# Kernel optimization log

Measured on AMD Instinct MI355X. Metric: run time of the kernel, lower is better.

Reference implementation:

```python
import math
import jax, jax.numpy as jnp
import numpy as np

N_HEAD = 32
LAYER_NUMBER = 10  # cancels out: beta*alibi*L + alpha*QK^T*L = alibi + QK^T/sqrt(d)


def build_alibi(seq_len, n_head, dtype):
    # Faithful port of BLOOM's build_alibi_tensor -> [n_head, 1, seq_len]
    cp2 = 2 ** math.floor(math.log2(n_head))
    base = 2.0 ** (-(2.0 ** -(math.log2(cp2) - 3)))
    slopes = base ** np.arange(1, 1 + cp2)
    if cp2 != n_head:
        extra_base = 2.0 ** (-(2.0 ** -(math.log2(2 * cp2) - 3)))
        num_rem = min(cp2, n_head - cp2)
        slopes = np.concatenate([slopes, extra_base ** np.arange(1, 1 + 2 * num_rem, 2)])
    alibi = slopes[:, None, None] * np.arange(seq_len)[None, None, :]
    return jnp.asarray(alibi, dtype)


def setup_inputs() -> dict:
    key = jax.random.key(0)
    ks = jax.random.split(key, 6)
    B, S, H = 4, 1024, 4096
    return {
        "hidden_states": jax.random.normal(ks[0], (B, S, H), jnp.float32),
        "residual": jax.random.normal(ks[1], (B, S, H), jnp.float32),
        "qkv_w": jax.random.normal(ks[2], (3 * H, H), jnp.float32) * 0.02,
        "qkv_b": jnp.zeros((3 * H,), jnp.float32),
        "dense_w": jax.random.normal(ks[3], (H, H), jnp.float32) * 0.02,
        "dense_b": jnp.zeros((H,), jnp.float32),
    }


def reference(hidden_states, residual, qkv_w, qkv_b, dense_w, dense_b):
    B, S, H = hidden_states.shape
    nh = N_HEAD
    d = H // nh
    # fused qkv projection: [B,S,3H] -> [B,S,nh,3d] -> split
    mixed = (hidden_states @ qkv_w.T + qkv_b).reshape(B, S, nh, 3 * d)
    q, k, v = jnp.split(mixed, 3, axis=-1)  # each [B,S,nh,d]

    alibi = build_alibi(S, nh, hidden_states.dtype)  # [nh,1,S]
    # beta*alibi + alpha*QK^T, then *layer_number in scaled softmax == alibi + QK^T/sqrt(d)
    scores = jnp.einsum("bqhd,bkhd->bhqk", q, k) / math.sqrt(d) + alibi[None]  # [B,nh,S,S]

    causal = jnp.tril(jnp.ones((S, S), bool))  # [S,S], True = attend
    scores = jnp.where(causal, scores, jnp.asarray(-10000.0, scores.dtype))
    # softmax in fp32 (attention_softmax_in_fp32), then zero masked entries like *(~padded_causal_mask)
    probs = jax.nn.softmax(scores.astype(jnp.float32), axis=-1) * causal
    probs = probs.astype(v.dtype)

    ctx = jnp.einsum("bhqk,bkhd->bqhd", probs, v).reshape(B, S, H)
    out = ctx @ dense_w.T + dense_b + residual  # dropout_add with p=0 / eval
    return out
```

## Files before the change

### kernel.cpp

```cpp
#include <hip/hip_runtime.h>
#include <hip/hip_bf16.h>

typedef __attribute__((ext_vector_type(8))) short bf16x8;
typedef __attribute__((ext_vector_type(4))) short short4v;
typedef __attribute__((ext_vector_type(4))) float f32x4;

#define MFMA16(A, B, C) __builtin_amdgcn_mfma_f32_16x16x32_bf16((A), (B), (C), 0, 0, 0)
#define GLDS16(g, l)                                                            \
  __builtin_amdgcn_global_load_lds(                                             \
      (const __attribute__((address_space(1))) void*)(g),                       \
      (__attribute__((address_space(3))) void*)(l), 16, 0, 0)

__device__ __forceinline__ short f2bf(float f) {
  union { float f; unsigned u; } v; v.f = f;
  return (short)((v.u + 0x7fffu + ((v.u >> 16) & 1u)) >> 16);
}

__device__ __forceinline__ void blk_barrier() {
  asm volatile("" ::: "memory");
  __builtin_amdgcn_s_barrier();
  asm volatile("" ::: "memory");
}

__global__ __launch_bounds__(256) void cvt_kernel(const float* __restrict__ in,
                                                  short* __restrict__ out, int n4) {
  int i = blockIdx.x * 256 + threadIdx.x;
  const int stride = gridDim.x * 256;
  for (; i < n4; i += stride) {
    f32x4 v = ((const f32x4*)in)[i];
    short4v o;
    o[0] = f2bf(v[0]); o[1] = f2bf(v[1]); o[2] = f2bf(v[2]); o[3] = f2bf(v[3]);
    ((short4v*)out)[i] = o;
  }
}

__global__ __launch_bounds__(512, 2) void gemm_bt8(const short* __restrict__ A,
                                                   const short* __restrict__ B,
                                                   const float* __restrict__ bias,
                                                   const float* __restrict__ resid,
                                                   short* __restrict__ Cb,
                                                   float* __restrict__ Cf,
                                                   int Mtiles, int Nn, int K, int mode) {
  __shared__ short sA[2][2][8192];
  __shared__ short sB[2][2][8192];
  const int tid = threadIdx.x;
  const int w = tid >> 6, l = tid & 63;
  const int wm = w >> 2, wn = w & 3;
  const int fr = l & 15, g4 = l >> 4, sx = l & 7;

  const int nwg = gridDim.x;
  const int qq = nwg >> 3, rr = nwg & 7;
  const int xcd = blockIdx.x & 7, sub = blockIdx.x >> 3;
  const int swz = (xcd < rr ? xcd * (qq + 1) : rr * (qq + 1) + (xcd - rr) * qq) + sub;
  const int rowBase = (swz % Mtiles) * 256;
  const int colBase = (swz / Mtiles) * 256;

  const int NT = K >> 6;
  const int swcol = ((l & 7) ^ (l >> 3)) * 8;
  const short* Ag = A + (size_t)(rowBase + w * 8 + (l >> 3)) * K + swcol;
  const short* Bg = B + (size_t)(colBase + w * 8 + (l >> 3)) * K + swcol;
  const size_t q1 = (size_t)64 * K;
  const size_t hh = (size_t)128 * K;

#define STAGE_A(buf, h, ko)                                     \
  GLDS16(Ag + (h) * hh + (ko), &sA[buf][h][w * 512]);           \
  GLDS16(Ag + (h) * hh + q1 + (ko), &sA[buf][h][(8 + w) * 512]);
#define STAGE_B(buf, h, ko)                                     \
  GLDS16(Bg + (h) * hh + (ko), &sB[buf][h][w * 512]);           \
  GLDS16(Bg + (h) * hh + q1 + (ko), &sB[buf][h][(8 + w) * 512]);
#define RD_A(buf, m, ks) \
  (*(const bf16x8*)&sA[buf][wm][(((m) * 16 + fr) << 6) + ((((ks) * 4 + g4) ^ sx) << 3)])
#define RD_B(buf, nf, ks) \
  (*(const bf16x8*)&sB[buf][wn >> 1][((((wn & 1) * 64) + (nf) * 16 + fr) << 6) + ((((ks) * 4 + g4) ^ sx) << 3)])

  f32x4 acc[8][4];
#pragma unroll
  for (int m = 0; m < 8; m++)
#pragma unroll
    for (int n = 0; n < 4; n++) acc[m][n] = (f32x4)(0.0f);

  STAGE_A(0, 0, 0); STAGE_A(0, 1, 0);
  STAGE_B(0, 0, 0); STAGE_B(0, 1, 0);

  for (int t = 0; t < NT; ++t) {
    const int cur = t & 1, nxt = cur ^ 1;
    const size_t ko = (size_t)(t + 1) << 6;
    bf16x8 bfr[4][2], af[2][2];
    if (t + 1 < NT) {
      STAGE_A(nxt, 0, ko);
      asm volatile("s_waitcnt vmcnt(2)" ::: "memory");
    } else {
      asm volatile("s_waitcnt vmcnt(0)" ::: "memory");
    }
    blk_barrier();
#pragma unroll
    for (int nf = 0; nf < 4; nf++) {
      bfr[nf][0] = RD_B(cur, nf, 0);
      bfr[nf][1] = RD_B(cur, nf, 1);
    }
    af[0][0] = RD_A(cur, 0, 0); af[0][1] = RD_A(cur, 0, 1);
    af[1][0] = RD_A(cur, 1, 0); af[1][1] = RD_A(cur, 1, 1);
    __builtin_amdgcn_s_setprio(1);
#pragma unroll
    for (int mi = 0; mi < 2; mi++)
#pragma unroll
      for (int nf = 0; nf < 4; nf++) {
        acc[mi][nf] = MFMA16(af[mi][0], bfr[nf][0], acc[mi][nf]);
        acc[mi][nf] = MFMA16(af[mi][1], bfr[nf][1], acc[mi][nf]);
      }
    __builtin_amdgcn_s_setprio(0);
    blk_barrier();
#pragma unroll
    for (int p = 1; p < 4; p++) {
      af[0][0] = RD_A(cur, 2 * p, 0);     af[0][1] = RD_A(cur, 2 * p, 1);
      af[1][0] = RD_A(cur, 2 * p + 1, 0); af[1][1] = RD_A(cur, 2 * p + 1, 1);
      if (t + 1 < NT) {
        if (p == 1)      { STAGE_A(nxt, 1, ko); }
        else if (p == 2) { STAGE_B(nxt, 0, ko); }
        else             { STAGE_B(nxt, 1, ko); }
      }
      blk_barrier();
      __builtin_amdgcn_s_setprio(1);
#pragma unroll
      for (int mi = 0; mi < 2; mi++)
#pragma unroll
        for (int nf = 0; nf < 4; nf++) {
          acc[2 * p + mi][nf] = MFMA16(af[mi][0], bfr[nf][0], acc[2 * p + mi][nf]);
          acc[2 * p + mi][nf] = MFMA16(af[mi][1], bfr[nf][1], acc[2 * p + mi][nf]);
        }
      __builtin_amdgcn_s_setprio(0);
      blk_barrier();
    }
  }

#pragma unroll
  for (int m = 0; m < 8; m++) {
    const int row0 = rowBase + wm * 128 + m * 16 + g4 * 4;
#pragma unroll
    for (int n = 0; n < 4; n++) {
      const int col = colBase + wn * 64 + n * 16 + fr;
      const float bc = bias[col];
#pragma unroll
      for (int j = 0; j < 4; j++) {
        const size_t idx = (size_t)(row0 + j) * Nn + col;
        const float v = acc[m][n][j] + bc;
        if (mode == 0) Cb[idx] = f2bf(v);
        else Cf[idx] = v + resid[idx];
      }
    }
  }
#undef STAGE_A
#undef STAGE_B
#undef RD_A
#undef RD_B
}

__global__ __launch_bounds__(256) void vtrans_kernel(const short* __restrict__ mixed,
                                                     short* __restrict__ vt) {
  __shared__ short tl[64][132];
  const int tid = threadIdx.x;
  const int st = blockIdx.x;
  const int bh = blockIdx.y;
  const int b = bh >> 5, h = bh & 31;
  const short* src = mixed + (size_t)(b * 1024 + st * 64) * 12288 + h * 384 + 256;
#pragma unroll
  for (int it = 0; it < 8; it++) {
    int idx = (tid + it * 256) * 4;
    int row = idx >> 7, col = idx & 127;
    *(short4v*)&tl[row][col] = *(const short4v*)(src + row * 12288 + col);
  }
  __syncthreads();
  short* dst = vt + (size_t)bh * 128 * 1024 + st * 64;
#pragma unroll
  for (int it = 0; it < 8; it++) {
    int o = (tid + it * 256) * 4;
    int d = o >> 6, t4 = o & 63;
    short4v w;
    w[0] = tl[t4][d]; w[1] = tl[t4 + 1][d]; w[2] = tl[t4 + 2][d]; w[3] = tl[t4 + 3][d];
    *(short4v*)(dst + d * 1024 + t4) = w;
  }
}

__global__ __launch_bounds__(256, 2) void attn_kernel(const short* __restrict__ mixed,
                                                      const short* __restrict__ vt,
                                                      short* __restrict__ ctx) {
  __shared__ short sK[2][64 * 128];
  __shared__ short sV[2][128 * 64];
  __shared__ unsigned p_lds[4][16 * 36];
  const int tid = threadIdx.x;
  const int w = tid >> 6, l = tid & 63;
  const int g = l >> 4, f = l & 15, f7 = l & 7;

  const int bidx = blockIdx.x;
  const int xcd = bidx & 7, idx = bidx >> 3;
  const int bh = (xcd << 4) | (idx >> 4);
  const int qt = idx & 15;
  const int b = bh >> 5, h = bh & 31;
  const int qw = qt * 64 + w * 16;
  const float scale = 0.08838834764831845f;
  const float slope = exp2f(-0.25f * (float)(h + 1));

  const short* qptr = mixed + (size_t)b * 1024 * 12288 + h * 384;
  const short* kptr = qptr + 128;
  const short* vtp = vt + (size_t)bh * 128 * 1024;

  bf16x8 qf[4];
  {
    const short* qrow = qptr + (size_t)(qw + f) * 12288 + (g << 3);
#pragma unroll
    for (int ks = 0; ks < 4; ks++) qf[ks] = *(const bf16x8*)(qrow + ks * 32);
  }

#define STAGE_K(buf, kt)                                                        \
  {                                                                             \
    _Pragma("unroll") for (int c4 = 0; c4 < 4; c4++) {                          \
      const int c = c4 * 4 + w;                                                 \
      const int r = c * 4 + (l >> 4);                                           \
      GLDS16(kptr + (size_t)((kt) + r) * 12288 + (((l & 15) ^ (r & 7)) << 3),   \
             &sK[buf][c << 9]);                                                 \
    }                                                                           \
  }
#define STAGE_V(buf, kt)                                                        \
  {                                                                             \
    _Pragma("unroll") for (int c4 = 0; c4 < 4; c4++) {                          \
      const int c = c4 * 4 + w;                                                 \
      const int r = c * 8 + (l >> 3);                                           \
      GLDS16(vtp + (size_t)r * 1024 + (kt) + (((l & 7) ^ (r & 7)) << 3),        \
             &sV[buf][c << 9]);                                                 \
    }                                                                           \
  }

  f32x4 acc[8];
#pragma unroll
  for (int n = 0; n < 8; n++) acc[n] = (f32x4)(0.0f);
  float mrun = -1e30f, lrun = 0.0f;
  const int q = qw + f;
  unsigned* pw = p_lds[w];

  const int TT = qt + 1;
  STAGE_K(0, 0);
  STAGE_V(0, 0);

  for (int t = 0; t < TT; ++t) {
    const int cur = t & 1, nxt = cur ^ 1;
    const int kt = t << 6;
    if (t + 1 < TT) {
      STAGE_K(nxt, kt + 64);
      STAGE_V(nxt, kt + 64);
      asm volatile("s_waitcnt vmcnt(8)" ::: "memory");
    } else {
      asm volatile("s_waitcnt vmcnt(0)" ::: "memory");
    }
    blk_barrier();

    f32x4 s[4];
#pragma unroll
    for (int ksub = 0; ksub < 4; ksub++) {
      s[ksub] = (f32x4)(0.0f);
      const int r = ksub * 16 + f;
#pragma unroll
      for (int ks = 0; ks < 4; ks++) {
        bf16x8 kf = *(const bf16x8*)&sK[cur][(r << 7) + ((((ks << 2) + g) ^ f7) << 3)];
        s[ksub] = MFMA16(kf, qf[ks], s[ksub]);
      }
    }

    float ev[4][4];
    float tmax = -1e30f;
#pragma unroll
    for (int ksub = 0; ksub < 4; ksub++)
#pragma unroll
      for (int j = 0; j < 4; j++) {
        const int k = kt + ksub * 16 + g * 4 + j;
        float v = s[ksub][j] * scale + slope * (float)k;
        if (k > q) v = -1e30f;
        ev[ksub][j] = v;
        tmax = fmaxf(tmax, v);
      }
    tmax = fmaxf(tmax, __shfl_xor(tmax, 16));
    tmax = fmaxf(tmax, __shfl_xor(tmax, 32));
    const float mnew = fmaxf(mrun, tmax);
    const float asc = __expf(mrun - mnew);
    float psum = 0.0f;
    unsigned* pr = pw + f * 36;
#pragma unroll
    for (int ksub = 0; ksub < 4; ksub++) {
      float e0 = __expf(ev[ksub][0] - mnew);
      float e1 = __expf(ev[ksub][1] - mnew);
      float e2 = __expf(ev[ksub][2] - mnew);
      float e3 = __expf(ev[ksub][3] - mnew);
      psum += (e0 + e1) + (e2 + e3);
      unsigned w0 = (unsigned)(unsigned short)f2bf(e0) |
                    ((unsigned)(unsigned short)f2bf(e1) << 16);
      unsigned w1 = (unsigned)(unsigned short)f2bf(e2) |
                    ((unsigned)(unsigned short)f2bf(e3) << 16);
      pr[ksub * 8 + g * 2] = w0;
      pr[ksub * 8 + g * 2 + 1] = w1;
    }
    psum += __shfl_xor(psum, 16);
    psum += __shfl_xor(psum, 32);
    lrun = lrun * asc + psum;
    mrun = mnew;

    float ascB[4];
#pragma unroll
    for (int j = 0; j < 4; j++) ascB[j] = __shfl(asc, 20 * g + j);
#pragma unroll
    for (int n = 0; n < 8; n++)
#pragma unroll
      for (int j = 0; j < 4; j++) acc[n][j] *= ascB[j];

    bf16x8 pa0 = *(const bf16x8*)(pw + f * 36 + (g << 2));
    bf16x8 pa1 = *(const bf16x8*)(pw + f * 36 + 16 + (g << 2));
#pragma unroll
    for (int n = 0; n < 8; n++) {
      const int dr = (n << 4) + f;
      bf16x8 vf0 = *(const bf16x8*)&sV[cur][(dr << 6) + ((g ^ f7) << 3)];
      acc[n] = MFMA16(pa0, vf0, acc[n]);
      bf16x8 vf1 = *(const bf16x8*)&sV[cur][(dr << 6) + (((4 + g) ^ f7) << 3)];
      acc[n] = MFMA16(pa1, vf1, acc[n]);
    }
    blk_barrier();
  }

  const float linv = 1.0f / lrun;
  float invB[4];
#pragma unroll
  for (int j = 0; j < 4; j++) invB[j] = __shfl(linv, 20 * g + j);
  const int trow = b * 1024 + qw + (g << 2);
#pragma unroll
  for (int n = 0; n < 8; n++) {
    const int col = h * 128 + (n << 4) + f;
#pragma unroll
    for (int j = 0; j < 4; j++)
      ctx[(size_t)(trow + j) * 4096 + col] = f2bf(acc[n][j] * invB[j]);
  }
#undef STAGE_K
#undef STAGE_V
}

extern "C" void kernel_launch(void* const* d_in, const int* in_sizes, int n_in,
                              void* d_out, int out_size, void* d_ws, size_t ws_size,
                              hipStream_t stream) {
  const float* hs = (const float*)d_in[0];
  const float* resid = (const float*)d_in[1];
  const float* qkv_w = (const float*)d_in[2];
  const float* qkv_b = (const float*)d_in[3];
  const float* dense_w = (const float*)d_in[4];
  const float* dense_b = (const float*)d_in[5];
  float* out = (float*)d_out;

  short* hs_b = (short*)d_ws;
  short* wqkv_b = hs_b + (size_t)16777216;
  short* wd_b = wqkv_b + (size_t)50331648;
  short* mixed = wd_b + (size_t)16777216;
  short* vt = wqkv_b;
  short* ctx = hs_b;

  cvt_kernel<<<1024, 256, 0, stream>>>(hs, hs_b, 16777216 / 4);
  cvt_kernel<<<1024, 256, 0, stream>>>(qkv_w, wqkv_b, 50331648 / 4);
  cvt_kernel<<<1024, 256, 0, stream>>>(dense_w, wd_b, 16777216 / 4);
  gemm_bt8<<<dim3(48 * 16), 512, 0, stream>>>(hs_b, wqkv_b, qkv_b, nullptr,
                                              mixed, nullptr, 16, 12288, 4096, 0);
  vtrans_kernel<<<dim3(16, 128), 256, 0, stream>>>(mixed, vt);
  attn_kernel<<<2048, 256, 0, stream>>>(mixed, vt, ctx);
  gemm_bt8<<<dim3(16 * 16), 512, 0, stream>>>(ctx, wd_b, dense_b, resid,
                                              nullptr, out, 16, 4096, 4096, 1);
}
```

Before: 820.6 us.

## Issue all next-tile staging up front and double-buffer A fragments in GEMM loop

Moves all global-to-LDS staging for the next K tile to the start of the iteration and waits with vmcnt(8), replacing the staggered staging spread across sub-phases. The inner loop now prefetches the next pair of A fragments from LDS into registers while the current MFMAs run, and drops one barrier per iteration. The aim is to overlap LDS reads with MFMA work and cut synchronisation. The cost is higher register pressure from the extra fragments and a burst of outstanding global loads.

```diff
diff --git a/kernel.cpp b/kernel.cpp
--- a/kernel.cpp
+++ b/kernel.cpp
@@ -85,14 +85,16 @@
   for (int t = 0; t < NT; ++t) {
     const int cur = t & 1, nxt = cur ^ 1;
     const size_t ko = (size_t)(t + 1) << 6;
-    bf16x8 bfr[4][2], af[2][2];
     if (t + 1 < NT) {
-      STAGE_A(nxt, 0, ko);
-      asm volatile("s_waitcnt vmcnt(2)" ::: "memory");
+      STAGE_A(nxt, 0, ko); STAGE_A(nxt, 1, ko);
+      STAGE_B(nxt, 0, ko); STAGE_B(nxt, 1, ko);
+      asm volatile("s_waitcnt vmcnt(8)" ::: "memory");
     } else {
       asm volatile("s_waitcnt vmcnt(0)" ::: "memory");
     }
     blk_barrier();
+
+    bf16x8 bfr[4][2], af[2][2];
 #pragma unroll
     for (int nf = 0; nf < 4; nf++) {
       bfr[nf][0] = RD_B(cur, nf, 0);
@@ -100,35 +102,28 @@
     }
     af[0][0] = RD_A(cur, 0, 0); af[0][1] = RD_A(cur, 0, 1);
     af[1][0] = RD_A(cur, 1, 0); af[1][1] = RD_A(cur, 1, 1);
-    __builtin_amdgcn_s_setprio(1);
-#pragma unroll
-    for (int mi = 0; mi < 2; mi++)
-#pragma unroll
-      for (int nf = 0; nf < 4; nf++) {
-        acc[mi][nf] = MFMA16(af[mi][0], bfr[nf][0], acc[mi][nf]);
-        acc[mi][nf] = MFMA16(af[mi][1], bfr[nf][1], acc[mi][nf]);
-      }
-    __builtin_amdgcn_s_setprio(0);
-    blk_barrier();
-#pragma unroll
-    for (int p = 1; p < 4; p++) {
-      af[0][0] = RD_A(cur, 2 * p, 0);     af[0][1] = RD_A(cur, 2 * p, 1);
-      af[1][0] = RD_A(cur, 2 * p + 1, 0); af[1][1] = RD_A(cur, 2 * p + 1, 1);
-      if (t + 1 < NT) {
-        if (p == 1)      { STAGE_A(nxt, 1, ko); }
-        else if (p == 2) { STAGE_B(nxt, 0, ko); }
-        else             { STAGE_B(nxt, 1, ko); }
-      }
-      blk_barrier();
+
+#pragma unroll
+    for (int p = 0; p < 4; p++) {
+      bf16x8 afn[2][2];
+      if (p < 3) {
+        afn[0][0] = RD_A(cur, 2 * p + 2, 0); afn[0][1] = RD_A(cur, 2 * p + 2, 1);
+        afn[1][0] = RD_A(cur, 2 * p + 3, 0); afn[1][1] = RD_A(cur, 2 * p + 3, 1);
+      }
       __builtin_amdgcn_s_setprio(1);
 #pragma unroll
-      for (int mi = 0; mi < 2; mi++)
-#pragma unroll
-        for (int nf = 0; nf < 4; nf++) {
-          acc[2 * p + mi][nf] = MFMA16(af[mi][0], bfr[nf][0], acc[2 * p + mi][nf]);
-          acc[2 * p + mi][nf] = MFMA16(af[mi][1], bfr[nf][1], acc[2 * p + mi][nf]);
-        }
+      for (int ks2 = 0; ks2 < 2; ks2++)
+#pragma unroll
+        for (int mi = 0; mi < 2; mi++)
+#pragma unroll
+          for (int nf = 0; nf < 4; nf++)
+            acc[2 * p + mi][nf] =
+                MFMA16(af[mi][ks2], bfr[nf][ks2], acc[2 * p + mi][nf]);
       __builtin_amdgcn_s_setprio(0);
+      if (p < 3) {
+        af[0][0] = afn[0][0]; af[0][1] = afn[0][1];
+        af[1][0] = afn[1][0]; af[1][1] = afn[1][1];
+      }
       blk_barrier();
     }
   }
```

New measurement: 918.4 us. 1.12x slower.
